# Kernel optimization log

Hardware: AMD Instinct MI355X
Metric: run time of the kernel (lower is better)

## Reference

```python
import jax, jax.numpy as jnp
import numpy as np

B, S, D = 4, 2048, 1024


def setup_inputs() -> dict:
    key = jax.random.key(0)
    ks = jax.random.split(key, 11)
    sc = 0.02
    f32 = jnp.float32
    return {
        "x1": jax.random.normal(ks[0], (B, S, D), f32),
        "x2": jax.random.normal(ks[1], (B, S, D), f32),
        "x3": jax.random.normal(ks[2], (B, S, D), f32),
        # Stacked per-modality projection weights, stored (in, out) so y = x @ W + b
        "Wq": jax.random.normal(ks[3], (3, D, D), f32) * sc,
        "bq": jax.random.normal(ks[4], (3, D), f32) * sc,
        "Wk": jax.random.normal(ks[5], (3, D, D), f32) * sc,
        "bk": jax.random.normal(ks[6], (3, D), f32) * sc,
        "Wv": jax.random.normal(ks[7], (3, D, D), f32) * sc,
        "bv": jax.random.normal(ks[8], (3, D), f32) * sc,
        "Wo": jax.random.normal(ks[9], (3, 2 * D, D), f32) * sc,
        "bo": jax.random.normal(ks[10], (3, D), f32) * sc,
    }


def reference(x1, x2, x3, Wq, bq, Wk, bk, Wv, bv, Wo, bo):
    x = jnp.stack([x1, x2, x3])                      # (3, B, S, D)
    q = jnp.einsum('mbsd,mde->mbse', x, Wq) + bq[:, None, None, :]
    k = jnp.einsum('mbsd,mde->mbse', x, Wk) + bk[:, None, None, :]
    v = jnp.einsum('mbsd,mde->mbse', x, Wv) + bv[:, None, None, :]
    scale = 1.0 / jnp.sqrt(jnp.asarray(x.shape[-1], x.dtype))
    # self-scores per modality: q_i @ k_i^T
    scores = jnp.einsum('mbsd,mbtd->mbst', q, k) * scale   # (3, B, S, S)
    attn = jax.nn.softmax(scores, axis=-1)
    # context_i = attn_i @ v_{(i+1) mod 3}  (1->2, 2->3, 3->1); dropout is eval-mode identity
    v_next = jnp.roll(v, shift=-1, axis=0)
    ctx = jnp.einsum('mbst,mbtd->mbsd', attn, v_next)      # (3, B, S, D)
    comb = jnp.concatenate([x, ctx], axis=-1)              # (3, B, S, 2D)
    out = jnp.einsum('mbsf,mfd->mbsd', comb, Wo) + bo[:, None, None, :]
    global_feature = jnp.concatenate([out[0], out[1], out[2]], axis=1)  # (B, 3S, D)
    return out[0], out[1], out[2], global_feature
```

## Files before the change

### kernel.cpp

```cpp
#include <hip/hip_runtime.h>
#include <hip/hip_bf16.h>

typedef __bf16 bf16_t;
typedef __bf16 bf16x8 __attribute__((ext_vector_type(8)));
typedef float f32x4 __attribute__((ext_vector_type(4)));

typedef __attribute__((address_space(1))) unsigned int as1_uint;
typedef __attribute__((address_space(3))) unsigned int as3_uint;

#define Bsz 4
#define Ssz 2048
#define Dsz 1024
#define BSD (Bsz * Ssz * Dsz)
#define SCALE_ 0.03125f

__device__ __forceinline__ void gll16(const void* g, void* l) {
  __builtin_amdgcn_global_load_lds((const as1_uint*)g, (as3_uint*)l, 16, 0, 0);
}

__device__ __forceinline__ unsigned bfbits(float f) {
  union { bf16_t h; unsigned short u; } c;
  c.h = (bf16_t)f;
  return (unsigned)c.u;
}

__device__ __forceinline__ ushort4 pack4(const f32x4 v, const float4 b) {
  ushort4 u;
  u.x = (unsigned short)bfbits(v[0] + b.x);
  u.y = (unsigned short)bfbits(v[1] + b.y);
  u.z = (unsigned short)bfbits(v[2] + b.z);
  u.w = (unsigned short)bfbits(v[3] + b.w);
  return u;
}

__device__ __forceinline__ void mf8(f32x4 acc[8][4], int ib, int jb,
                                    const bf16x8 b[2], const bf16x8 a[4]) {
  __builtin_amdgcn_s_setprio(1);
#pragma unroll
  for (int i = 0; i < 4; ++i)
#pragma unroll
    for (int j = 0; j < 2; ++j)
      acc[ib + i][jb + j] = __builtin_amdgcn_mfma_f32_16x16x32_bf16(
          b[j], a[i], acc[ib + i][jb + j], 0, 0, 0);
  __builtin_amdgcn_s_setprio(0);
}

#define PHASE_BAR() do {                                   \
    asm volatile("s_waitcnt lgkmcnt(0)" ::: "memory");     \
    __builtin_amdgcn_sched_barrier(0);                     \
    __builtin_amdgcn_s_barrier();                          \
    __builtin_amdgcn_sched_barrier(0);                     \
  } while (0)

__device__ __forceinline__ void gemm_core256(char* smem,
    const bf16_t* A, const bf16_t* A2, int ks, int lda,
    const bf16_t* Bt, int ldb, int KT, f32x4 acc[8][4]) {
  const int tid = threadIdx.x;
  const int wave = tid >> 6, lane = tid & 63;
  const int quad = lane >> 4, m16 = lane & 15;
  const int wm = wave >> 2, wn = wave & 3;
  const int swz = ((quad ^ ((m16 >> 1) & 3)) << 4);
  const int Ab = ((wm * 128 + m16) << 6) + swz;
  const int Bb = 32768 + ((wn * 64 + m16) << 6) + swz;

  const int srow = tid >> 2;
  const int sg = (((tid & 3) ^ ((srow >> 1) & 3)) << 3);
  const size_t aoff = (size_t)srow * lda + sg;
  const size_t boff = (size_t)srow * ldb + sg;
  const size_t astep = (size_t)128 * lda;
  const size_t bstep = (size_t)128 * ldb;
  char* ldsW = smem + (wave << 10);

  auto stageA = [&](const bf16_t* As, int sb, int kh) {
    const bf16_t* s = As + aoff + kh * 32;
    char* d = ldsW + sb + kh * 16384;
    gll16(s, d);
    gll16(s + astep, d + 8192);
  };
  auto stageB = [&](const bf16_t* Bs, int sb, int kh) {
    const bf16_t* s = Bs + boff + kh * 32;
    char* d = ldsW + sb + 32768 + kh * 16384;
    gll16(s, d);
    gll16(s + bstep, d + 8192);
  };

#pragma unroll
  for (int t0 = 0; t0 < 2; ++t0) {
    const bf16_t* As = (t0 < ks) ? (A + t0 * 64) : (A2 + (t0 - ks) * 64);
    const bf16_t* Bs = Bt + t0 * 64;
    const int sb = t0 << 16;
    stageB(Bs, sb, 0); stageB(Bs, sb, 1);
    stageA(As, sb, 0); stageA(As, sb, 1);
  }

  bf16x8 a0[4], a1[4], b00[2], b01[2], b10[2], b11[2];

#pragma unroll 1
  for (int t = 0; t < KT; ++t) {
    const int cur = (t & 1) << 16;
    const int tp = (t + 2 < KT) ? (t + 2) : (KT - 1);
    const bf16_t* As = (tp < ks) ? (A + tp * 64) : (A2 + (tp - ks) * 64);
    const bf16_t* Bs = Bt + tp * 64;
    const char* sbp = smem + cur;

    asm volatile("s_waitcnt vmcnt(8)" ::: "memory");
    __builtin_amdgcn_sched_barrier(0);
    __builtin_amdgcn_s_barrier();
    __builtin_amdgcn_sched_barrier(0);

#pragma unroll
    for (int i = 0; i < 4; ++i) a0[i] = *(const bf16x8*)(sbp + (Ab + i * 1024));
#pragma unroll
    for (int j = 0; j < 2; ++j) b00[j] = *(const bf16x8*)(sbp + (Bb + j * 1024));
    mf8(acc, 0, 0, b00, a0);

#pragma unroll
    for (int i = 0; i < 4; ++i) a1[i] = *(const bf16x8*)(sbp + (16384 + Ab + i * 1024));
#pragma unroll
    for (int j = 0; j < 2; ++j) b01[j] = *(const bf16x8*)(sbp + (16384 + Bb + j * 1024));
    mf8(acc, 0, 0, b01, a1);

#pragma unroll
    for (int j = 0; j < 2; ++j) b10[j] = *(const bf16x8*)(sbp + (Bb + 2048 + j * 1024));
    mf8(acc, 0, 2, b10, a0);
    PHASE_BAR();

    stageB(Bs, cur, 0);
#pragma unroll
    for (int j = 0; j < 2; ++j) b11[j] = *(const bf16x8*)(sbp + (16384 + Bb + 2048 + j * 1024));
    mf8(acc, 0, 2, b11, a1);
    PHASE_BAR();

    stageB(Bs, cur, 1);
#pragma unroll
    for (int i = 0; i < 4; ++i) a0[i] = *(const bf16x8*)(sbp + (Ab + 4096 + i * 1024));
    mf8(acc, 4, 0, b00, a0);
    PHASE_BAR();

    stageA(As, cur, 0);
#pragma unroll
    for (int i = 0; i < 4; ++i) a1[i] = *(const bf16x8*)(sbp + (16384 + Ab + 4096 + i * 1024));
    mf8(acc, 4, 0, b01, a1);
    PHASE_BAR();

    stageA(As, cur, 1);
    mf8(acc, 4, 2, b10, a0);

    mf8(acc, 4, 2, b11, a1);
  }

  asm volatile("s_waitcnt vmcnt(0)" ::: "memory");
  __builtin_amdgcn_sched_barrier(0);
}

#define EPI_VARS                                               \
  const int tid = threadIdx.x, lane = tid & 63, wave = tid >> 6; \
  const int quad = lane >> 4, m16 = lane & 15;                 \
  const int wm = wave >> 2, wn = wave & 3;                     \
  (void)tid; (void)quad; (void)m16; (void)wm; (void)wn;
#define MLOC(ip) (wm * 128 + (((ip) >> 2) << 6) + (((ip) & 3) << 4) + m16)
#define NLOC(jp) (wn * 64 + (((jp) >> 1) << 5) + (((jp) & 1) << 4) + (quad << 2))

__global__ __launch_bounds__(512, 2)
void gemm_bt_bf16(const bf16_t* __restrict__ A, long long sAz, int lda,
                  const bf16_t* __restrict__ Bt, long long sBz, int ldb,
                  bf16_t* __restrict__ C, long long sCz, int ldc,
                  int K, int rollB) {
  __shared__ __attribute__((aligned(16))) char smem[131072];
  const int z = blockIdx.z;
  int zb = z;
  if (rollB) { const int m = z >> 2, b = z & 3; zb = ((m + 1) % 3) * Bsz + b; }
  const bf16_t* Az = A + (long long)z * sAz + (size_t)blockIdx.y * 256 * lda;
  const bf16_t* Bz = Bt + (long long)zb * sBz + (size_t)blockIdx.x * 256 * ldb;
  f32x4 acc[8][4];
  const f32x4 zero = {0.f, 0.f, 0.f, 0.f};
#pragma unroll
  for (int i = 0; i < 8; ++i)
#pragma unroll
    for (int j = 0; j < 4; ++j) acc[i][j] = zero;

  gemm_core256(smem, Az, Az, 1 << 30, lda, Bz, ldb, K / 64, acc);

  EPI_VARS;
  bf16_t* Cz = C + (long long)z * sCz;
  const float4 zb4 = {0.f, 0.f, 0.f, 0.f};
#pragma unroll
  for (int ip = 0; ip < 8; ++ip) {
    const size_t M = (size_t)blockIdx.y * 256 + MLOC(ip);
#pragma unroll
    for (int jp = 0; jp < 4; ++jp) {
      const int N = blockIdx.x * 256 + NLOC(jp);
      *(ushort4*)(Cz + M * ldc + N) = pack4(acc[ip][jp], zb4);
    }
  }
}

__global__ __launch_bounds__(512, 2)
void gemm_qkv(const bf16_t* __restrict__ xb, const bf16_t* __restrict__ Wqkvt,
              const float* __restrict__ bq, const float* __restrict__ bk,
              const float* __restrict__ bvp,
              bf16_t* __restrict__ Q, bf16_t* __restrict__ Kb, bf16_t* __restrict__ Vt) {
  __shared__ __attribute__((aligned(16))) char smem[131072];
  const int m = blockIdx.z;
  const int x = blockIdx.x;
  const int which = x >> 2;
  const bf16_t* Az = xb + (size_t)m * BSD + (size_t)blockIdx.y * 256 * Dsz;
  const bf16_t* Bz = Wqkvt + (size_t)m * 3145728 + (size_t)x * 262144;
  f32x4 acc[8][4];
  const f32x4 zero = {0.f, 0.f, 0.f, 0.f};
#pragma unroll
  for (int i = 0; i < 8; ++i)
#pragma unroll
    for (int j = 0; j < 4; ++j) acc[i][j] = zero;

  gemm_core256(smem, Az, Az, 1 << 30, Dsz, Bz, Dsz, 16, acc);

  EPI_VARS;
  const int dseg0 = (x & 3) * 256;
  const float* bb = (which == 0 ? bq : which == 1 ? bk : bvp) + m * Dsz;

  if (which < 2) {
    bf16_t* Cz = (which == 0 ? Q : Kb) + (size_t)m * BSD;
#pragma unroll
    for (int jp = 0; jp < 4; ++jp) {
      const int N = NLOC(jp);
      const float4 b4 = *(const float4*)(bb + dseg0 + N);
#pragma unroll
      for (int ip = 0; ip < 8; ++ip) {
        const size_t M = (size_t)blockIdx.y * 256 + MLOC(ip);
        *(ushort4*)(Cz + M * Dsz + dseg0 + N) = pack4(acc[ip][jp], b4);
      }
    }
  } else {
    unsigned short* T = (unsigned short*)smem;
    const int b = blockIdx.y >> 3;
    const int s0 = (blockIdx.y & 7) * 256;
    bf16_t* Vz = Vt + ((size_t)(m * 4 + b) * 1024 + dseg0) * (size_t)Ssz;
#pragma unroll
    for (int nh = 0; nh < 2; ++nh) {
      __syncthreads();
      if ((wn >> 1) == nh) {
#pragma unroll
        for (int jp = 0; jp < 4; ++jp) {
          const int Nh = ((wn & 1) << 6) + (((jp) >> 1) << 5) + (((jp) & 1) << 4) + (quad << 2);
          const float4 b4 = *(const float4*)(bb + dseg0 + nh * 128 + Nh);
          const float bia[4] = {b4.x, b4.y, b4.z, b4.w};
#pragma unroll
          for (int ip = 0; ip < 8; ++ip) {
            const int M = MLOC(ip);
#pragma unroll
            for (int r = 0; r < 4; ++r)
              T[(Nh + r) * 264 + M] = (unsigned short)bfbits(acc[ip][jp][r] + bia[r]);
          }
        }
      }
      __syncthreads();
#pragma unroll
      for (int e = 0; e < 8; ++e) {
        const int c = e * 512 + tid;
        const int n = c >> 5, mc = (c & 31) * 8;
        *(uint4*)(Vz + (size_t)(nh * 128 + n) * Ssz + s0 + mc) =
            *(const uint4*)(T + n * 264 + mc);
      }
    }
  }
}

__global__ __launch_bounds__(512, 2)
void gemm_out(const bf16_t* __restrict__ xb, const bf16_t* __restrict__ ctx,
              const bf16_t* __restrict__ Wot, const float* __restrict__ bo,
              float* __restrict__ out) {
  __shared__ __attribute__((aligned(16))) char smem[131072];
  const int m = blockIdx.z;
  const bf16_t* Az = xb + (size_t)m * BSD + (size_t)blockIdx.y * 256 * Dsz;
  const bf16_t* A2z = ctx + (size_t)m * BSD + (size_t)blockIdx.y * 256 * Dsz;
  const bf16_t* Bz = Wot + (size_t)m * (Dsz * 2 * Dsz) + (size_t)blockIdx.x * 256 * (2 * Dsz);
  f32x4 acc[8][4];
  const f32x4 zero = {0.f, 0.f, 0.f, 0.f};
#pragma unroll
  for (int i = 0; i < 8; ++i)
#pragma unroll
    for (int j = 0; j < 4; ++j) acc[i][j] = zero;

  gemm_core256(smem, Az, A2z, 16, Dsz, Bz, 2 * Dsz, 32, acc);

  EPI_VARS;
  const float* bz = bo + m * Dsz;
#pragma unroll
  for (int ip = 0; ip < 8; ++ip) {
    const int M = blockIdx.y * 256 + MLOC(ip);
    const int b = M >> 11, s = M & 2047;
    float* o1 = out + (size_t)m * BSD + (size_t)M * Dsz;
    float* o2 = out + (size_t)3 * BSD + (size_t)b * (3 * Ssz * Dsz) + (size_t)(m * Ssz + s) * Dsz;
#pragma unroll
    for (int jp = 0; jp < 4; ++jp) {
      const int N = blockIdx.x * 256 + NLOC(jp);
      const float4 b4 = *(const float4*)(bz + N);
      float4 o;
      o.x = acc[ip][jp][0] + b4.x; o.y = acc[ip][jp][1] + b4.y;
      o.z = acc[ip][jp][2] + b4.z; o.w = acc[ip][jp][3] + b4.w;
      *(float4*)(o1 + N) = o;
      *(float4*)(o2 + N) = o;
    }
  }
}

__global__ __launch_bounds__(256)
void cvt_x(const float* __restrict__ x1, const float* __restrict__ x2,
           const float* __restrict__ x3, bf16_t* __restrict__ xb) {
  const size_t i = ((size_t)blockIdx.x * 256 + threadIdx.x) * 4;
  const float* src;
  size_t off;
  if (i < (size_t)BSD)          { src = x1; off = i; }
  else if (i < (size_t)2 * BSD) { src = x2; off = i - BSD; }
  else                          { src = x3; off = i - (size_t)2 * BSD; }
  const float4 v = *(const float4*)(src + off);
  union { bf16_t h[4]; uint2 u; } o;
  o.h[0] = (bf16_t)v.x; o.h[1] = (bf16_t)v.y; o.h[2] = (bf16_t)v.z; o.h[3] = (bf16_t)v.w;
  *(uint2*)(xb + i) = o.u;
}

__global__ __launch_bounds__(256)
void transpose_to_bf16(const float* __restrict__ in, bf16_t* __restrict__ out,
                       int ldin, int ldout, long long sIn, long long sOut) {
  __shared__ bf16_t Ts[64][65];
  const int t = threadIdx.x;
  const long long z = blockIdx.z;
  const float* inz = in + z * sIn;
  bf16_t* outz = out + z * sOut;
  const int r0 = blockIdx.y << 6, c0 = blockIdx.x << 6;
#pragma unroll
  for (int e = 0; e < 4; ++e) {
    const int idx = (e * 256 + t) * 4;
    const int rr = idx >> 6, cc = idx & 63;
    const float4 v = *(const float4*)(inz + (size_t)(r0 + rr) * ldin + (c0 + cc));
    Ts[rr][cc] = (bf16_t)v.x; Ts[rr][cc + 1] = (bf16_t)v.y;
    Ts[rr][cc + 2] = (bf16_t)v.z; Ts[rr][cc + 3] = (bf16_t)v.w;
  }
  __syncthreads();
#pragma unroll
  for (int e = 0; e < 4; ++e) {
    const int idx = (e * 256 + t) * 4;
    const int oc = idx >> 6, orr = idx & 63;
    union { bf16_t h[4]; uint2 u; } o4;
    o4.h[0] = Ts[orr][oc]; o4.h[1] = Ts[orr + 1][oc];
    o4.h[2] = Ts[orr + 2][oc]; o4.h[3] = Ts[orr + 3][oc];
    *(uint2*)(outz + (size_t)(c0 + oc) * ldout + (r0 + orr)) = o4.u;
  }
}

__global__ __launch_bounds__(256)
void softmax_rows(bf16_t* __restrict__ Sc) {
  const size_t row = blockIdx.x;
  uint4* p = (uint4*)(Sc + row * Ssz);
  const int t = threadIdx.x;
  const int lane = t & 63, wave = t >> 6;
  uint4 u = p[t];
  float v[8];
  v[0] = __uint_as_float(u.x << 16); v[1] = __uint_as_float(u.x & 0xffff0000u);
  v[2] = __uint_as_float(u.y << 16); v[3] = __uint_as_float(u.y & 0xffff0000u);
  v[4] = __uint_as_float(u.z << 16); v[5] = __uint_as_float(u.z & 0xffff0000u);
  v[6] = __uint_as_float(u.w << 16); v[7] = __uint_as_float(u.w & 0xffff0000u);

  float mx = v[0];
#pragma unroll
  for (int i = 1; i < 8; ++i) mx = fmaxf(mx, v[i]);
  for (int o = 32; o > 0; o >>= 1) mx = fmaxf(mx, __shfl_xor(mx, o));
  __shared__ float redm[4], reds[4];
  if (lane == 0) redm[wave] = mx;
  __syncthreads();
  mx = fmaxf(fmaxf(redm[0], redm[1]), fmaxf(redm[2], redm[3]));

  float s = 0.f;
#pragma unroll
  for (int i = 0; i < 8; ++i) { v[i] = __expf((v[i] - mx) * SCALE_); s += v[i]; }
  for (int o = 32; o > 0; o >>= 1) s += __shfl_xor(s, o);
  if (lane == 0) reds[wave] = s;
  __syncthreads();
  s = reds[0] + reds[1] + reds[2] + reds[3];
  const float inv = 1.0f / s;
#pragma unroll
  for (int i = 0; i < 8; ++i) v[i] *= inv;

  u.x = bfbits(v[0]) | (bfbits(v[1]) << 16);
  u.y = bfbits(v[2]) | (bfbits(v[3]) << 16);
  u.z = bfbits(v[4]) | (bfbits(v[5]) << 16);
  u.w = bfbits(v[6]) | (bfbits(v[7]) << 16);
  p[t] = u;
}

extern "C" void kernel_launch(void* const* d_in, const int* in_sizes, int n_in,
                              void* d_out, int out_size, void* d_ws, size_t ws_size,
                              hipStream_t stream) {
  const float* x1 = (const float*)d_in[0];
  const float* x2 = (const float*)d_in[1];
  const float* x3 = (const float*)d_in[2];
  const float* Wq = (const float*)d_in[3];
  const float* bq = (const float*)d_in[4];
  const float* Wk = (const float*)d_in[5];
  const float* bk = (const float*)d_in[6];
  const float* Wv = (const float*)d_in[7];
  const float* bv = (const float*)d_in[8];
  const float* Wo = (const float*)d_in[9];
  const float* bo = (const float*)d_in[10];

  char* ws = (char*)d_ws;
  bf16_t* xb    = (bf16_t*)(ws + 0);
  bf16_t* Wqkvt = (bf16_t*)(ws + 50331648);
  bf16_t* Wot   = (bf16_t*)(ws + 69206016);
  bf16_t* Q     = (bf16_t*)(ws + 81788928);
  bf16_t* Kb    = (bf16_t*)(ws + 132120576);
  bf16_t* Vt    = (bf16_t*)(ws + 182452224);
  bf16_t* Sc    = (bf16_t*)d_out;
  bf16_t* ctx   = Q;

  cvt_x<<<24576, 256, 0, stream>>>(x1, x2, x3, xb);
  transpose_to_bf16<<<dim3(16, 16, 3), 256, 0, stream>>>(Wq, Wqkvt + 0,       1024, 1024, 1048576LL, 3145728LL);
  transpose_to_bf16<<<dim3(16, 16, 3), 256, 0, stream>>>(Wk, Wqkvt + 1048576, 1024, 1024, 1048576LL, 3145728LL);
  transpose_to_bf16<<<dim3(16, 16, 3), 256, 0, stream>>>(Wv, Wqkvt + 2097152, 1024, 1024, 1048576LL, 3145728LL);
  transpose_to_bf16<<<dim3(16, 32, 3), 256, 0, stream>>>(Wo, Wot, 1024, 2048, 2097152LL, 2097152LL);
  gemm_qkv<<<dim3(12, 32, 3), 512, 0, stream>>>(xb, Wqkvt, bq, bk, bv, Q, Kb, Vt);
  gemm_bt_bf16<<<dim3(8, 8, 12), 512, 0, stream>>>(Q, 2097152LL, Dsz, Kb, 2097152LL, Dsz, Sc, 4194304LL, Ssz, Dsz, 0);
  softmax_rows<<<24576, 256, 0, stream>>>(Sc);
  gemm_bt_bf16<<<dim3(4, 8, 12), 512, 0, stream>>>(Sc, 4194304LL, Ssz, Vt, 2097152LL, Ssz, ctx, 2097152LL, Dsz, Ssz, 1);
  gemm_out<<<dim3(4, 32, 3), 512, 0, stream>>>(xb, ctx, Wot, bo, (float*)d_out);
}
```

Measured before the change: 921.9 us.

## Remap GEMM tiles per XCD for L2 locality and regroup MFMA phases

All three GEMM kernels now remap their linear block index so that blocks landing on the same XCD (round-robin by index mod 8) work on neighbouring A-row and B-column tiles. This is meant to raise per-XCD L2 reuse of the shared operands. The inner K loop is also restructured: LDS fragments are loaded in larger groups into separate registers, the MFMAs run in pairs under one raised priority, and the number of intra-iteration barriers drops from four to two. The cost is higher VGPR pressure from the extra fragment arrays, which could hurt occupancy or scheduling at the 2-blocks-per-CU bound.

```diff
diff --git a/kernel.cpp b/kernel.cpp
--- a/kernel.cpp
+++ b/kernel.cpp
@@ -35,14 +35,12 @@
 
 __device__ __forceinline__ void mf8(f32x4 acc[8][4], int ib, int jb,
                                     const bf16x8 b[2], const bf16x8 a[4]) {
-  __builtin_amdgcn_s_setprio(1);
 #pragma unroll
   for (int i = 0; i < 4; ++i)
 #pragma unroll
     for (int j = 0; j < 2; ++j)
       acc[ib + i][jb + j] = __builtin_amdgcn_mfma_f32_16x16x32_bf16(
           b[j], a[i], acc[ib + i][jb + j], 0, 0, 0);
-  __builtin_amdgcn_s_setprio(0);
 }
 
 #define PHASE_BAR() do {                                   \
@@ -93,8 +91,6 @@
     stageA(As, sb, 0); stageA(As, sb, 1);
   }
 
-  bf16x8 a0[4], a1[4], b00[2], b01[2], b10[2], b11[2];
-
 #pragma unroll 1
   for (int t = 0; t < KT; ++t) {
     const int cur = (t & 1) << 16;
@@ -108,45 +104,51 @@
     __builtin_amdgcn_s_barrier();
     __builtin_amdgcn_sched_barrier(0);
 
-#pragma unroll
-    for (int i = 0; i < 4; ++i) a0[i] = *(const bf16x8*)(sbp + (Ab + i * 1024));
+    bf16x8 aA[4], aB[4], aC[4], aD[4], b00[2], b01[2], b10[2], b11[2];
+
+#pragma unroll
+    for (int i = 0; i < 4; ++i) aA[i] = *(const bf16x8*)(sbp + (Ab + i * 1024));
 #pragma unroll
     for (int j = 0; j < 2; ++j) b00[j] = *(const bf16x8*)(sbp + (Bb + j * 1024));
-    mf8(acc, 0, 0, b00, a0);
-
-#pragma unroll
-    for (int i = 0; i < 4; ++i) a1[i] = *(const bf16x8*)(sbp + (16384 + Ab + i * 1024));
+#pragma unroll
+    for (int i = 0; i < 4; ++i) aB[i] = *(const bf16x8*)(sbp + (16384 + Ab + i * 1024));
 #pragma unroll
     for (int j = 0; j < 2; ++j) b01[j] = *(const bf16x8*)(sbp + (16384 + Bb + j * 1024));
-    mf8(acc, 0, 0, b01, a1);
+    __builtin_amdgcn_s_setprio(1);
+    mf8(acc, 0, 0, b00, aA);
+    mf8(acc, 0, 0, b01, aB);
+    __builtin_amdgcn_s_setprio(0);
 
 #pragma unroll
     for (int j = 0; j < 2; ++j) b10[j] = *(const bf16x8*)(sbp + (Bb + 2048 + j * 1024));
-    mf8(acc, 0, 2, b10, a0);
+#pragma unroll
+    for (int j = 0; j < 2; ++j) b11[j] = *(const bf16x8*)(sbp + (16384 + Bb + 2048 + j * 1024));
+    __builtin_amdgcn_s_setprio(1);
+    mf8(acc, 0, 2, b10, aA);
+    mf8(acc, 0, 2, b11, aB);
+    __builtin_amdgcn_s_setprio(0);
+
     PHASE_BAR();
 
     stageB(Bs, cur, 0);
-#pragma unroll
-    for (int j = 0; j < 2; ++j) b11[j] = *(const bf16x8*)(sbp + (16384 + Bb + 2048 + j * 1024));
-    mf8(acc, 0, 2, b11, a1);
+    stageB(Bs, cur, 1);
+#pragma unroll
+    for (int i = 0; i < 4; ++i) aC[i] = *(const bf16x8*)(sbp + (Ab + 4096 + i * 1024));
+#pragma unroll
+    for (int i = 0; i < 4; ++i) aD[i] = *(const bf16x8*)(sbp + (16384 + Ab + 4096 + i * 1024));
+    __builtin_amdgcn_s_setprio(1);
+    mf8(acc, 4, 0, b00, aC);
+    mf8(acc, 4, 0, b01, aD);
+    __builtin_amdgcn_s_setprio(0);
+
     PHASE_BAR();
 
-    stageB(Bs, cur, 1);
-#pragma unroll
-    for (int i = 0; i < 4; ++i) a0[i] = *(const bf16x8*)(sbp + (Ab + 4096 + i * 1024));
-    mf8(acc, 4, 0, b00, a0);
-    PHASE_BAR();
-
     stageA(As, cur, 0);
-#pragma unroll
-    for (int i = 0; i < 4; ++i) a1[i] = *(const bf16x8*)(sbp + (16384 + Ab + 4096 + i * 1024));
-    mf8(acc, 4, 0, b01, a1);
-    PHASE_BAR();
-
     stageA(As, cur, 1);
-    mf8(acc, 4, 2, b10, a0);
-
-    mf8(acc, 4, 2, b11, a1);
+    __builtin_amdgcn_s_setprio(1);
+    mf8(acc, 4, 2, b10, aC);
+    mf8(acc, 4, 2, b11, aD);
+    __builtin_amdgcn_s_setprio(0);
   }
 
   asm volatile("s_waitcnt vmcnt(0)" ::: "memory");
@@ -165,13 +167,18 @@
 void gemm_bt_bf16(const bf16_t* __restrict__ A, long long sAz, int lda,
                   const bf16_t* __restrict__ Bt, long long sBz, int ldb,
                   bf16_t* __restrict__ C, long long sCz, int ldc,
-                  int K, int rollB) {
+                  int K, int rollB, int cxlog) {
   __shared__ __attribute__((aligned(16))) char smem[131072];
   const int z = blockIdx.z;
   int zb = z;
   if (rollB) { const int m = z >> 2, b = z & 3; zb = ((m + 1) % 3) * Bsz + b; }
-  const bf16_t* Az = A + (long long)z * sAz + (size_t)blockIdx.y * 256 * lda;
-  const bf16_t* Bz = Bt + (long long)zb * sBz + (size_t)blockIdx.x * 256 * ldb;
+  const int L = blockIdx.x + gridDim.x * blockIdx.y;
+  const int xcd = L & 7, loc = L >> 3;
+  const int cx = 1 << cxlog;
+  const int nx = ((xcd >> 2) << cxlog) + (loc & (cx - 1));
+  const int ny = ((xcd & 3) << 1) + (loc >> cxlog);
+  const bf16_t* Az = A + (long long)z * sAz + (size_t)ny * 256 * lda;
+  const bf16_t* Bz = Bt + (long long)zb * sBz + (size_t)nx * 256 * ldb;
   f32x4 acc[8][4];
   const f32x4 zero = {0.f, 0.f, 0.f, 0.f};
 #pragma unroll
@@ -186,10 +193,10 @@
   const float4 zb4 = {0.f, 0.f, 0.f, 0.f};
 #pragma unroll
   for (int ip = 0; ip < 8; ++ip) {
-    const size_t M = (size_t)blockIdx.y * 256 + MLOC(ip);
+    const size_t M = (size_t)ny * 256 + MLOC(ip);
 #pragma unroll
     for (int jp = 0; jp < 4; ++jp) {
-      const int N = blockIdx.x * 256 + NLOC(jp);
+      const int N = nx * 256 + NLOC(jp);
       *(ushort4*)(Cz + M * ldc + N) = pack4(acc[ip][jp], zb4);
     }
   }
@@ -202,9 +209,12 @@
               bf16_t* __restrict__ Q, bf16_t* __restrict__ Kb, bf16_t* __restrict__ Vt) {
   __shared__ __attribute__((aligned(16))) char smem[131072];
   const int m = blockIdx.z;
-  const int x = blockIdx.x;
+  const int L = blockIdx.x + 12 * blockIdx.y;
+  const int xcd = L & 7, loc = L >> 3;
+  const int x = loc % 12;
+  const int by = (xcd << 2) + loc / 12;
   const int which = x >> 2;
-  const bf16_t* Az = xb + (size_t)m * BSD + (size_t)blockIdx.y * 256 * Dsz;
+  const bf16_t* Az = xb + (size_t)m * BSD + (size_t)by * 256 * Dsz;
   const bf16_t* Bz = Wqkvt + (size_t)m * 3145728 + (size_t)x * 262144;
   f32x4 acc[8][4];
   const f32x4 zero = {0.f, 0.f, 0.f, 0.f};
@@ -227,14 +237,14 @@
       const float4 b4 = *(const float4*)(bb + dseg0 + N);
 #pragma unroll
       for (int ip = 0; ip < 8; ++ip) {
-        const size_t M = (size_t)blockIdx.y * 256 + MLOC(ip);
+        const size_t M = (size_t)by * 256 + MLOC(ip);
         *(ushort4*)(Cz + M * Dsz + dseg0 + N) = pack4(acc[ip][jp], b4);
       }
     }
   } else {
     unsigned short* T = (unsigned short*)smem;
-    const int b = blockIdx.y >> 3;
-    const int s0 = (blockIdx.y & 7) * 256;
+    const int b = by >> 3;
+    const int s0 = (by & 7) * 256;
     bf16_t* Vz = Vt + ((size_t)(m * 4 + b) * 1024 + dseg0) * (size_t)Ssz;
 #pragma unroll
     for (int nh = 0; nh < 2; ++nh) {
@@ -272,9 +282,13 @@
               float* __restrict__ out) {
   __shared__ __attribute__((aligned(16))) char smem[131072];
   const int m = blockIdx.z;
-  const bf16_t* Az = xb + (size_t)m * BSD + (size_t)blockIdx.y * 256 * Dsz;
-  const bf16_t* A2z = ctx + (size_t)m * BSD + (size_t)blockIdx.y * 256 * Dsz;
-  const bf16_t* Bz = Wot + (size_t)m * (Dsz * 2 * Dsz) + (size_t)blockIdx.x * 256 * (2 * Dsz);
+  const int L = blockIdx.x + 4 * blockIdx.y;
+  const int xcd = L & 7, loc = L >> 3;
+  const int nx = ((xcd >> 2) << 1) + (loc & 1);
+  const int ny = ((xcd & 3) << 3) + (loc >> 1);
+  const bf16_t* Az = xb + (size_t)m * BSD + (size_t)ny * 256 * Dsz;
+  const bf16_t* A2z = ctx + (size_t)m * BSD + (size_t)ny * 256 * Dsz;
+  const bf16_t* Bz = Wot + (size_t)m * (Dsz * 2 * Dsz) + (size_t)nx * 256 * (2 * Dsz);
   f32x4 acc[8][4];
   const f32x4 zero = {0.f, 0.f, 0.f, 0.f};
 #pragma unroll
@@ -288,13 +302,13 @@
   const float* bz = bo + m * Dsz;
 #pragma unroll
   for (int ip = 0; ip < 8; ++ip) {
-    const int M = blockIdx.y * 256 + MLOC(ip);
+    const int M = ny * 256 + MLOC(ip);
     const int b = M >> 11, s = M & 2047;
     float* o1 = out + (size_t)m * BSD + (size_t)M * Dsz;
     float* o2 = out + (size_t)3 * BSD + (size_t)b * (3 * Ssz * Dsz) + (size_t)(m * Ssz + s) * Dsz;
 #pragma unroll
     for (int jp = 0; jp < 4; ++jp) {
-      const int N = blockIdx.x * 256 + NLOC(jp);
+      const int N = nx * 256 + NLOC(jp);
       const float4 b4 = *(const float4*)(bz + N);
       float4 o;
       o.x = acc[ip][jp][0] + b4.x; o.y = acc[ip][jp][1] + b4.y;
@@ -420,8 +434,8 @@
   transpose_to_bf16<<<dim3(16, 16, 3), 256, 0, stream>>>(Wv, Wqkvt + 2097152, 1024, 1024, 1048576LL, 3145728LL);
   transpose_to_bf16<<<dim3(16, 32, 3), 256, 0, stream>>>(Wo, Wot, 1024, 2048, 2097152LL, 2097152LL);
   gemm_qkv<<<dim3(12, 32, 3), 512, 0, stream>>>(xb, Wqkvt, bq, bk, bv, Q, Kb, Vt);
-  gemm_bt_bf16<<<dim3(8, 8, 12), 512, 0, stream>>>(Q, 2097152LL, Dsz, Kb, 2097152LL, Dsz, Sc, 4194304LL, Ssz, Dsz, 0);
+  gemm_bt_bf16<<<dim3(8, 8, 12), 512, 0, stream>>>(Q, 2097152LL, Dsz, Kb, 2097152LL, Dsz, Sc, 4194304LL, Ssz, Dsz, 0, 2);
   softmax_rows<<<24576, 256, 0, stream>>>(Sc);
-  gemm_bt_bf16<<<dim3(4, 8, 12), 512, 0, stream>>>(Sc, 4194304LL, Ssz, Vt, 2097152LL, Ssz, ctx, 2097152LL, Dsz, Ssz, 1);
+  gemm_bt_bf16<<<dim3(4, 8, 12), 512, 0, stream>>>(Sc, 4194304LL, Ssz, Vt, 2097152LL, Ssz, ctx, 2097152LL, Dsz, Ssz, 1, 1);
   gemm_out<<<dim3(4, 32, 3), 512, 0, stream>>>(xb, ctx, Wot, bo, (float*)d_out);
 }
```

Result: no change. 908.3 us (-1.5%).
